# Kernel tuning notes

Measured on AMD Instinct MI355X. Metric: run time of the kernel, lower is better.

The kernel has to match this reference:

```python
import jax, jax.numpy as jnp
import numpy as np

EPS = 1e-6


def softmax_kernel_transformation(data, is_query, projection_matrix):
    # data: [B,L,H,D], projection_matrix: [M,D]
    d = data.shape[-1]
    m = projection_matrix.shape[0]
    data_normalizer = 1.0 / jnp.sqrt(jnp.sqrt(jnp.float32(d)))
    data = data_normalizer * data
    ratio = 1.0 / jnp.sqrt(jnp.float32(m))
    data_dash = jnp.einsum('blhd,md->blhm', data, projection_matrix)
    diag_data = jnp.sum(jnp.square(data), axis=-1, keepdims=True) / 2.0  # [B,L,H,1]
    if is_query:
        stab = jnp.max(data_dash, axis=-1, keepdims=True)  # per-position max over M
    else:
        stab = jnp.max(data_dash, axis=(1, 3), keepdims=True)  # max over L and M
    return ratio * (jnp.exp(data_dash - diag_data - stab) + EPS)


def causal_linear_attention(qp, kp, v):
    # qp,kp: [L,B,H,M]; v: [L,B,H,D]. Sequential prefix-sum recurrence (FAVOR+ causal).
    B, H, M = qp.shape[1], qp.shape[2], qp.shape[3]
    D = v.shape[-1]
    kv0 = jnp.zeros((B, H, M, D), dtype=v.dtype)
    ks0 = jnp.zeros((B, H, M), dtype=kp.dtype)

    def step(carry, inp):
        kv_sum, k_sum = carry
        q_t, k_t, v_t = inp  # [B,H,M], [B,H,M], [B,H,D]
        kv_sum = kv_sum + jnp.einsum('bhm,bhd->bhmd', k_t, v_t)
        k_sum = k_sum + k_t
        num_t = jnp.einsum('bhmd,bhm->bhd', kv_sum, q_t)  # numerator row
        den_t = jnp.einsum('bhm,bhm->bh', q_t, k_sum)     # normalizer row
        return (kv_sum, k_sum), (num_t, den_t)

    (_, _), (num, den) = jax.lax.scan(step, (kv0, ks0), (qp, kp, v))
    return num, den  # [L,B,H,D], [L,B,H]


def favor_attention(query, key, value, projection_matrix):
    query_prime = softmax_kernel_transformation(query, True, projection_matrix)   # [B,L,H,M]
    key_prime = softmax_kernel_transformation(key, False, projection_matrix)      # [B,L,H,M]
    qp = jnp.transpose(query_prime, (1, 0, 2, 3))  # [L,B,H,M]
    kp = jnp.transpose(key_prime, (1, 0, 2, 3))
    v = jnp.transpose(value, (1, 0, 2, 3))         # [L,B,H,D]
    num, den = causal_linear_attention(qp, kp, v)
    av = jnp.transpose(num, (1, 0, 2, 3))          # [B,L,H,D]
    norm = jnp.transpose(den, (1, 0, 2))[..., None]  # [B,L,H,1]
    return av / norm


def setup_inputs() -> dict:
    B, L, H, D, M = 2, 2048, 8, 64, 128
    root = jax.random.key(0)
    kq, kk, kv, kp = jax.random.split(root, 4)
    return {
        'query': jax.random.normal(kq, (B, L, H, D), dtype=jnp.float32),
        'key': jax.random.normal(kk, (B, L, H, D), dtype=jnp.float32),
        'value': jax.random.normal(kv, (B, L, H, D), dtype=jnp.float32),
        'projection_matrix': jax.random.normal(kp, (M, D), dtype=jnp.float32),
    }


def reference(query, key, value, projection_matrix):
    return favor_attention(query, key, value, projection_matrix)
```

## Files before the change

kernel.cpp:

```cpp
#include <hip/hip_runtime.h>
#include <math.h>

typedef __attribute__((ext_vector_type(8))) short short8;
typedef __attribute__((ext_vector_type(4))) float f32x4;
typedef __attribute__((ext_vector_type(4))) unsigned short u16x4;

constexpr int B_ = 2, L_ = 2048, H_ = 8, D_ = 64, M_ = 128;
constexpr int T_ = 64;
constexpr int C_ = L_ / T_;
constexpr float DN_ = 0.35355339059327373f;
constexpr float RATIO_ = 0.08838834764831845f;
constexpr float EPSV_ = 1e-6f;
constexpr float REPS_ = RATIO_ * EPSV_;
constexpr float KEPS_ = 64.0f * REPS_;

constexpr int XQ_ = 0, XK_ = 4608, PHO_ = 9216, VTO_ = 18432;
constexpr int QPST_ = 0, KPTO_ = 9216, KVSTO_ = 0;

__device__ inline unsigned short f2bf(float x) {
  const unsigned u = __float_as_uint(x);
  return (unsigned short)((u + 0x7fffu + ((u >> 16) & 1u)) >> 16);
}
__device__ inline float bf2f(unsigned short h) {
  return __uint_as_float(((unsigned)h) << 16);
}

__global__ __launch_bounds__(256, 3) void feat_kernel(
    const float* __restrict__ q, const float* __restrict__ k,
    const float* __restrict__ P, const float* __restrict__ v,
    unsigned short* __restrict__ qp16, unsigned short* __restrict__ kp16,
    unsigned short* __restrict__ kvc16, float* __restrict__ ksc,
    unsigned short* __restrict__ vt16, float* __restrict__ blockmax,
    float* __restrict__ vsum) {
  __shared__ __align__(16) unsigned short sm[23040];
  __shared__ float diagq_s[T_];
  __shared__ float diagk_s[T_];
  __shared__ float wred_s[2][T_];
  __shared__ float red4_s[4];

  const int sub = blockIdx.x;
  const int c = sub % C_, bh = sub / C_;
  const int b = bh >> 3, h = bh & 7;
  const int tid = threadIdx.x;
  const int w = tid >> 6, lane = tid & 63;
  const int l15 = lane & 15, l16 = lane >> 4;
  const int rblk = (w >> 1) * 32, cblk = (w & 1) * 64;

#define STAGE_X(xptr, XB, dg)                                                 \
  _Pragma("unroll") for (int it = 0; it < 4; ++it) {                          \
    const int i4 = tid + 256 * it;                                            \
    const int r = i4 >> 4, d0 = (i4 & 15) * 4;                                \
    f32x4 t4 = *reinterpret_cast<const f32x4*>(                               \
        &(xptr)[((size_t)(b * L_ + c * T_ + r) * H_ + h) * D_ + d0]);         \
    u16x4 hi;                                                                 \
    float sq = 0.f;                                                           \
    _Pragma("unroll") for (int j = 0; j < 4; ++j) {                           \
      const float xv = t4[j] * DN_;                                           \
      sq += xv * xv;                                                          \
      hi[j] = f2bf(xv);                                                       \
    }                                                                         \
    *reinterpret_cast<u16x4*>(&sm[(XB) + r * 72 + d0]) = hi;                  \
    _Pragma("unroll") for (int off = 1; off < 16; off <<= 1)                  \
        sq += __shfl_xor(sq, off, 64);                                        \
    if ((tid & 15) == 0) (dg)[r] = sq;                                        \
  }

#define DASH_MFMA(accv, XB)                                                   \
  _Pragma("unroll") for (int kk = 0; kk < 2; ++kk) {                          \
    short8 ah[2], bh8[4];                                                     \
    _Pragma("unroll") for (int ti = 0; ti < 2; ++ti)                          \
      ah[ti] = *reinterpret_cast<const short8*>(                              \
          &sm[(XB) + (rblk + ti * 16 + l15) * 72 + kk * 32 + l16 * 8]);       \
    _Pragma("unroll") for (int tj = 0; tj < 4; ++tj)                          \
      bh8[tj] = *reinterpret_cast<const short8*>(                             \
          &sm[PHO_ + (cblk + tj * 16 + l15) * 72 + kk * 32 + l16 * 8]);       \
    _Pragma("unroll") for (int ti = 0; ti < 2; ++ti)                          \
        _Pragma("unroll") for (int tj = 0; tj < 4; ++tj)                      \
            accv[ti][tj] = __builtin_amdgcn_mfma_f32_16x16x32_bf16(           \
                ah[ti], bh8[tj], accv[ti][tj], 0, 0, 0);                      \
  }

  STAGE_X(q, XQ_, diagq_s);
  STAGE_X(k, XK_, diagk_s);
  for (int i4 = tid; i4 < M_ * 16; i4 += 256) {
    const int m = i4 >> 4, d0 = (i4 & 15) * 4;
    const f32x4 t4 = *reinterpret_cast<const f32x4*>(&P[m * D_ + d0]);
    u16x4 hi;
#pragma unroll
    for (int j = 0; j < 4; ++j) hi[j] = f2bf(t4[j]);
    *reinterpret_cast<u16x4*>(&sm[PHO_ + m * 72 + d0]) = hi;
  }
#pragma unroll
  for (int it = 0; it < 4; ++it) {
    const int i4 = tid + 256 * it;
    const int t = i4 >> 4, d0 = (i4 & 15) * 4;
    const f32x4 t4 = *reinterpret_cast<const f32x4*>(
        &v[((size_t)(b * L_ + c * T_ + t) * H_ + h) * D_ + d0]);
#pragma unroll
    for (int j = 0; j < 4; ++j) sm[VTO_ + (d0 + j) * 72 + t] = f2bf(t4[j]);
  }
  __syncthreads();

  f32x4 accq[2][4], acck[2][4];
#pragma unroll
  for (int i = 0; i < 2; ++i)
#pragma unroll
    for (int j = 0; j < 4; ++j) {
      accq[i][j] = {0.f, 0.f, 0.f, 0.f};
      acck[i][j] = {0.f, 0.f, 0.f, 0.f};
    }
  DASH_MFMA(accq, XQ_);
  DASH_MFMA(acck, XK_);
  {
    float rmax[2][4];
#pragma unroll
    for (int ti = 0; ti < 2; ++ti)
#pragma unroll
      for (int j = 0; j < 4; ++j) {
        float m0 = fmaxf(fmaxf(accq[ti][0][j], accq[ti][1][j]),
                         fmaxf(accq[ti][2][j], accq[ti][3][j]));
#pragma unroll
        for (int off = 1; off < 16; off <<= 1)
          m0 = fmaxf(m0, __shfl_xor(m0, off, 64));
        rmax[ti][j] = m0;
      }
    if (l15 == 0) {
#pragma unroll
      for (int ti = 0; ti < 2; ++ti)
#pragma unroll
        for (int j = 0; j < 4; ++j)
          wred_s[w & 1][rblk + ti * 16 + l16 * 4 + j] = rmax[ti][j];
    }
  }
  {
    float bm = -INFINITY;
#pragma unroll
    for (int ti = 0; ti < 2; ++ti)
#pragma unroll
      for (int tj = 0; tj < 4; ++tj)
#pragma unroll
        for (int j = 0; j < 4; ++j) bm = fmaxf(bm, acck[ti][tj][j]);
#pragma unroll
    for (int off = 1; off < 64; off <<= 1)
      bm = fmaxf(bm, __shfl_xor(bm, off, 64));
    if (lane == 0) red4_s[w] = bm;
  }
  __syncthreads();

  const float lmax =
      fmaxf(fmaxf(red4_s[0], red4_s[1]), fmaxf(red4_s[2], red4_s[3]));
  if (tid == 0) blockmax[sub] = lmax;
#pragma unroll
  for (int ti = 0; ti < 2; ++ti)
#pragma unroll
    for (int j = 0; j < 4; ++j) {
      const int row = rblk + ti * 16 + l16 * 4 + j;
      const float sub2 =
          0.5f * diagq_s[row] + fmaxf(wred_s[0][row], wred_s[1][row]);
#pragma unroll
      for (int tj = 0; tj < 4; ++tj) {
        const int col = cblk + tj * 16 + l15;
        sm[QPST_ + row * 136 + col] =
            f2bf(RATIO_ * (expf(accq[ti][tj][j] - sub2) + EPSV_));
      }
    }
  {
    unsigned short* kpr = kp16 + ((size_t)bh * L_ + c * T_) * M_;
#pragma unroll
    for (int ti = 0; ti < 2; ++ti)
#pragma unroll
      for (int j = 0; j < 4; ++j) {
        const int row = rblk + ti * 16 + l16 * 4 + j;
        const float sub2 = 0.5f * diagk_s[row] + lmax;
#pragma unroll
        for (int tj = 0; tj < 4; ++tj) {
          const int col = cblk + tj * 16 + l15;
          const unsigned short us = f2bf(RATIO_ * expf(acck[ti][tj][j] - sub2));
          kpr[row * M_ + col] = us;
          sm[KPTO_ + col * 72 + row] = us;
        }
      }
  }
  __syncthreads();

  {
    unsigned short* outr = qp16 + ((size_t)bh * L_ + c * T_) * M_;
    for (int i8 = tid; i8 < T_ * 16; i8 += 256) {
      const int row = i8 >> 4, m0 = (i8 & 15) * 8;
      *reinterpret_cast<short8*>(&outr[row * M_ + m0]) =
          *reinterpret_cast<const short8*>(&sm[QPST_ + row * 136 + m0]);
    }
    unsigned short* vg = vt16 + (size_t)(bh * C_ + c) * (D_ * T_);
    for (int i8 = tid; i8 < D_ * 8; i8 += 256) {
      const int d = i8 >> 3, t0 = (i8 & 7) * 8;
      *reinterpret_cast<short8*>(&vg[d * T_ + t0]) =
          *reinterpret_cast<const short8*>(&sm[VTO_ + d * 72 + t0]);
    }
  }
  if (tid < M_) {
    float s = 0.f;
#pragma unroll
    for (int t8 = 0; t8 < 8; ++t8) {
      const short8 h8 =
          *reinterpret_cast<const short8*>(&sm[KPTO_ + tid * 72 + t8 * 8]);
#pragma unroll
      for (int j = 0; j < 8; ++j) s += bf2f((unsigned short)h8[j]);
    }
    ksc[(size_t)(bh * C_ + c) * M_ + tid] = s;
  }
  if (tid >= 128 && tid < 128 + D_) {
    const int d = tid - 128;
    float s = 0.f;
#pragma unroll
    for (int t8 = 0; t8 < 8; ++t8) {
      const short8 h8 =
          *reinterpret_cast<const short8*>(&sm[VTO_ + d * 72 + t8 * 8]);
#pragma unroll
      for (int j = 0; j < 8; ++j) s += bf2f((unsigned short)h8[j]);
    }
    vsum[(size_t)(bh * C_ + c) * D_ + d] = s;
  }
  f32x4 acc2[2][4];
#pragma unroll
  for (int i = 0; i < 2; ++i)
#pragma unroll
    for (int j = 0; j < 4; ++j) acc2[i][j] = {0.f, 0.f, 0.f, 0.f};
#pragma unroll
  for (int kk = 0; kk < 2; ++kk) {
    short8 av[2], bv[4];
#pragma unroll
    for (int ti = 0; ti < 2; ++ti)
      av[ti] = *reinterpret_cast<const short8*>(
          &sm[VTO_ + (rblk + ti * 16 + l15) * 72 + kk * 32 + l16 * 8]);
#pragma unroll
    for (int tj = 0; tj < 4; ++tj)
      bv[tj] = *reinterpret_cast<const short8*>(
          &sm[KPTO_ + (cblk + tj * 16 + l15) * 72 + kk * 32 + l16 * 8]);
#pragma unroll
    for (int ti = 0; ti < 2; ++ti)
#pragma unroll
      for (int tj = 0; tj < 4; ++tj)
        acc2[ti][tj] = __builtin_amdgcn_mfma_f32_16x16x32_bf16(
            av[ti], bv[tj], acc2[ti][tj], 0, 0, 0);
  }
  __syncthreads();
#pragma unroll
  for (int ti = 0; ti < 2; ++ti)
#pragma unroll
    for (int j = 0; j < 4; ++j) {
      const int row = rblk + ti * 16 + l16 * 4 + j;
#pragma unroll
      for (int tj = 0; tj < 4; ++tj) {
        const int col = cblk + tj * 16 + l15;
        sm[KVSTO_ + row * 136 + col] = f2bf(acc2[ti][tj][j]);
      }
    }
  __syncthreads();
  {
    unsigned short* ob = kvc16 + (size_t)(bh * C_ + c) * (M_ * D_);
    for (int i8 = tid; i8 < D_ * 16; i8 += 256) {
      const int d = i8 >> 4, m0 = (i8 & 15) * 8;
      *reinterpret_cast<short8*>(&ob[d * M_ + m0]) =
          *reinterpret_cast<const short8*>(&sm[KVSTO_ + d * 136 + m0]);
    }
  }
#undef STAGE_X
#undef DASH_MFMA
}

__global__ __launch_bounds__(256) void prefix_kernel(
    const unsigned short* __restrict__ kvc16,
    unsigned short* __restrict__ kvp16, float* __restrict__ ksc,
    const float* __restrict__ blockmax, const float* __restrict__ vsum) {
  __shared__ float bm_s[C_];
  __shared__ float sc_s[C_];
  __shared__ float vs_s[2][C_];
  const int bid = blockIdx.x;
  const int ej = bid & 31, bh = bid >> 5;
  if (threadIdx.x < C_) bm_s[threadIdx.x] = blockmax[bh * C_ + threadIdx.x];
  if (threadIdx.x >= 64 && threadIdx.x < 64 + 2 * C_) {
    const int t = threadIdx.x - 64;
    const int ld = t >> 5, cc = t & 31;
    vs_s[ld][cc] = vsum[(size_t)(bh * C_ + cc) * D_ + ej * 2 + ld];
  }
  __syncthreads();
  if (threadIdx.x < C_) {
    float km = -INFINITY;
#pragma unroll
    for (int cc = 0; cc < C_; ++cc) km = fmaxf(km, bm_s[cc]);
    sc_s[threadIdx.x] = expf(bm_s[threadIdx.x] - km);
  }
  __syncthreads();
  const int e = ej * 256 + threadIdx.x;
  const int dl = threadIdx.x >> 7;
  float vals[C_];
#pragma unroll
  for (int cc = 0; cc < C_; ++cc)
    vals[cc] = bf2f(kvc16[(size_t)(bh * C_ + cc) * (M_ * D_) + e]) * sc_s[cc] +
               REPS_ * vs_s[dl][cc];
  float run = 0.f;
#pragma unroll
  for (int cc = 0; cc < C_; ++cc) {
    const float t = vals[cc];
    vals[cc] = run;
    run += t;
  }
#pragma unroll
  for (int cc = 0; cc < C_; ++cc)
    kvp16[(size_t)(bh * C_ + cc) * (M_ * D_) + e] = f2bf(vals[cc]);
  if (ej == 0 && threadIdx.x < M_) {
    const int m = threadIdx.x;
    float ks[C_];
#pragma unroll
    for (int cc = 0; cc < C_; ++cc)
      ks[cc] = ksc[(size_t)(bh * C_ + cc) * M_ + m] * sc_s[cc] + KEPS_;
    float rs = 0.f;
#pragma unroll
    for (int cc = 0; cc < C_; ++cc) {
      const float t = ks[cc];
      ks[cc] = rs;
      rs += t;
    }
#pragma unroll
    for (int cc = 0; cc < C_; ++cc)
      ksc[(size_t)(bh * C_ + cc) * M_ + m] = ks[cc];
  }
}

__global__ __launch_bounds__(256, 3) void intra_kernel(
    const unsigned short* __restrict__ qp16,
    const unsigned short* __restrict__ kp16,
    const unsigned short* __restrict__ vt16,
    const unsigned short* __restrict__ kvp16, const float* __restrict__ ksp,
    const float* __restrict__ blockmax, float* __restrict__ out) {
  __shared__ __align__(16) unsigned short qp_s[T_][136];
  __shared__ __align__(16) unsigned short kp_s[T_][136];
  __shared__ __align__(16) unsigned short S_s[T_][72];
  __shared__ float ksp_s[M_];
  __shared__ float denp_s[4][T_];
  __shared__ float den_s[T_];
  __shared__ float qsum_s[T_];
  __shared__ float bm_s[C_];

  const int bid = blockIdx.x;
  const int c = bid % C_, bh = bid / C_;
  const int b = bh >> 3, h = bh & 7;
  const int tid = threadIdx.x;
  const int w = tid >> 6, lane = tid & 63;
  const int l15 = lane & 15, l16 = lane >> 4;
  const int dblk = (w & 1) * 32;

  const unsigned short* qpt = qp16 + ((size_t)bh * L_ + c * T_) * M_;
  const unsigned short* kpt = kp16 + ((size_t)bh * L_ + c * T_) * M_;
  const unsigned short* kvt = kvp16 + (size_t)(bh * C_ + c) * (M_ * D_);
  const unsigned short* vg = vt16 + (size_t)(bh * C_ + c) * (D_ * T_);

  short8 vtr[2][2], kvr[4][2];
#pragma unroll
  for (int kk = 0; kk < 2; ++kk)
#pragma unroll
    for (int tj = 0; tj < 2; ++tj)
      vtr[kk][tj] = *reinterpret_cast<const short8*>(
          &vg[(dblk + tj * 16 + l15) * T_ + kk * 32 + l16 * 8]);
#pragma unroll
  for (int kk = 0; kk < 4; ++kk)
#pragma unroll
    for (int tj = 0; tj < 2; ++tj)
      kvr[kk][tj] = *reinterpret_cast<const short8*>(
          &kvt[(dblk + tj * 16 + l15) * M_ + kk * 32 + l16 * 8]);

  if (tid < C_) bm_s[tid] = blockmax[bh * C_ + tid];
  for (int i8 = tid; i8 < T_ * 16; i8 += 256) {
    const int r = i8 >> 4, m0 = (i8 & 15) * 8;
    *reinterpret_cast<short8*>(&qp_s[r][m0]) =
        *reinterpret_cast<const short8*>(&qpt[r * M_ + m0]);
    *reinterpret_cast<short8*>(&kp_s[r][m0]) =
        *reinterpret_cast<const short8*>(&kpt[r * M_ + m0]);
  }
  if (tid < M_) ksp_s[tid] = ksp[(size_t)(bh * C_ + c) * M_ + tid];
  __syncthreads();

  {
    const int row = w * 16 + (lane >> 2), mseg = (lane & 3) * 32;
    float p = 0.f;
#pragma unroll
    for (int u = 0; u < 4; ++u) {
      const short8 h8 =
          *reinterpret_cast<const short8*>(&qp_s[row][mseg + u * 8]);
#pragma unroll
      for (int j = 0; j < 8; ++j) p += bf2f((unsigned short)h8[j]);
    }
    p += __shfl_xor(p, 1, 64);
    p += __shfl_xor(p, 2, 64);
    if ((lane & 3) == 0) qsum_s[row] = p;
  }
  __syncthreads();

  float km = -INFINITY;
#pragma unroll
  for (int cc = 0; cc < C_; ++cc) km = fmaxf(km, bm_s[cc]);
  const float sc = expf(bm_s[c] - km);

  const int rblk = (w >> 1) * 32, cblk = (w & 1) * 32;
  f32x4 Sacc[2][2];
#pragma unroll
  for (int i = 0; i < 2; ++i)
#pragma unroll
    for (int j = 0; j < 2; ++j) Sacc[i][j] = {0.f, 0.f, 0.f, 0.f};

#pragma unroll
  for (int kk = 0; kk < 4; ++kk) {
    short8 af[2], bf[2];
#pragma unroll
    for (int ti = 0; ti < 2; ++ti)
      af[ti] = *reinterpret_cast<const short8*>(
          &qp_s[rblk + ti * 16 + l15][kk * 32 + l16 * 8]);
#pragma unroll
    for (int tj = 0; tj < 2; ++tj)
      bf[tj] = *reinterpret_cast<const short8*>(
          &kp_s[cblk + tj * 16 + l15][kk * 32 + l16 * 8]);
#pragma unroll
    for (int ti = 0; ti < 2; ++ti)
#pragma unroll
      for (int tj = 0; tj < 2; ++tj)
        Sacc[ti][tj] = __builtin_amdgcn_mfma_f32_16x16x32_bf16(
            af[ti], bf[tj], Sacc[ti][tj], 0, 0, 0);
  }
#pragma unroll
  for (int ti = 0; ti < 2; ++ti)
#pragma unroll
    for (int tj = 0; tj < 2; ++tj)
#pragma unroll
      for (int j = 0; j < 4; ++j) {
        const int row = rblk + ti * 16 + l16 * 4 + j;
        const int col = cblk + tj * 16 + l15;
        const float add = REPS_ * qsum_s[row];
        const float sv = (col <= row) ? Sacc[ti][tj][j] * sc + add : 0.f;
        S_s[row][col] = f2bf(sv);
      }
  __syncthreads();

  {
    const int t = lane;
    float p = 0.f;
    if (w == 0) {
      for (int tp = 0; tp < 32; ++tp) p += bf2f(S_s[t][tp]);
    } else if (w == 1) {
      for (int tp = 32; tp < 64; ++tp) p += bf2f(S_s[t][tp]);
    } else if (w == 2) {
      for (int m = 0; m < 64; ++m) p += bf2f(qp_s[t][m]) * ksp_s[m];
    } else {
      for (int m = 64; m < 128; ++m) p += bf2f(qp_s[t][m]) * ksp_s[m];
    }
    denp_s[w][t] = p;
  }
  __syncthreads();
  if (tid < T_)
    den_s[tid] =
        denp_s[0][tid] + denp_s[1][tid] + denp_s[2][tid] + denp_s[3][tid];
  __syncthreads();

  f32x4 Nacc[2][2];
#pragma unroll
  for (int i = 0; i < 2; ++i)
#pragma unroll
    for (int j = 0; j < 2; ++j) Nacc[i][j] = {0.f, 0.f, 0.f, 0.f};

#pragma unroll
  for (int kk = 0; kk < 2; ++kk) {
    short8 af[2];
#pragma unroll
    for (int ti = 0; ti < 2; ++ti)
      af[ti] = *reinterpret_cast<const short8*>(
          &S_s[rblk + ti * 16 + l15][kk * 32 + l16 * 8]);
#pragma unroll
    for (int ti = 0; ti < 2; ++ti)
#pragma unroll
      for (int tj = 0; tj < 2; ++tj)
        Nacc[ti][tj] = __builtin_amdgcn_mfma_f32_16x16x32_bf16(
            af[ti], vtr[kk][tj], Nacc[ti][tj], 0, 0, 0);
  }
#pragma unroll
  for (int kk = 0; kk < 4; ++kk) {
    short8 af[2];
#pragma unroll
    for (int ti = 0; ti < 2; ++ti)
      af[ti] = *reinterpret_cast<const short8*>(
          &qp_s[rblk + ti * 16 + l15][kk * 32 + l16 * 8]);
#pragma unroll
    for (int ti = 0; ti < 2; ++ti)
#pragma unroll
      for (int tj = 0; tj < 2; ++tj)
        Nacc[ti][tj] = __builtin_amdgcn_mfma_f32_16x16x32_bf16(
            af[ti], kvr[kk][tj], Nacc[ti][tj], 0, 0, 0);
  }

#pragma unroll
  for (int ti = 0; ti < 2; ++ti)
#pragma unroll
    for (int j = 0; j < 4; ++j) {
      const int row = rblk + ti * 16 + l16 * 4 + j;
      const float r = 1.f / den_s[row];
      float* orow = out + ((size_t)(b * L_ + c * T_ + row) * H_ + h) * D_;
#pragma unroll
      for (int tj = 0; tj < 2; ++tj) {
        const int col = dblk + tj * 16 + l15;
        orow[col] = Nacc[ti][tj][j] * r;
      }
    }
}

extern "C" void kernel_launch(void* const* d_in, const int* in_sizes, int n_in,
                              void* d_out, int out_size, void* d_ws,
                              size_t ws_size, hipStream_t stream) {
  const float* q = (const float*)d_in[0];
  const float* k = (const float*)d_in[1];
  const float* v = (const float*)d_in[2];
  const float* P = (const float*)d_in[3];
  float* out = (float*)d_out;

  float* ws = (float*)d_ws;
  float* blockmax = ws;
  float* ksp = blockmax + 512;
  float* vsum = ksp + (size_t)B_ * H_ * C_ * M_;
  unsigned short* qp16 = (unsigned short*)(vsum + (size_t)B_ * H_ * C_ * D_);
  unsigned short* kp16 = qp16 + (size_t)B_ * H_ * L_ * M_;
  unsigned short* kvc16 = kp16 + (size_t)B_ * H_ * L_ * M_;
  unsigned short* kvp16 = kvc16 + (size_t)B_ * H_ * C_ * D_ * M_;
  unsigned short* vt16 = kvp16 + (size_t)B_ * H_ * C_ * D_ * M_;

  feat_kernel<<<B_ * H_ * C_, 256, 0, stream>>>(q, k, P, v, qp16, kp16, kvc16,
                                                ksp, vt16, blockmax, vsum);
  prefix_kernel<<<B_ * H_ * 32, 256, 0, stream>>>(kvc16, kvp16, ksp, blockmax,
                                                  vsum);
  intra_kernel<<<B_ * H_ * C_, 256, 0, stream>>>(qp16, kp16, vt16, kvp16, ksp,
                                                 blockmax, out);
}
```

Before: 41.61 us.

## Recompute query/key features in intra kernel instead of round-tripping through global memory

The feature kernel no longer computes query features or writes the bf16 qp/kp tensors to global memory. The intra kernel now reloads raw q, k and P, recomputes both projections with MFMA, applies the exponentials, and forms the per-row q sums in registers. This removes the global write and read of two L×M bf16 feature tensors per head and lets the feature kernel use less LDS with higher occupancy. In exchange, the key projection is computed twice and the intra kernel does more work and needs more LDS.

```diff
diff --git a/kernel.cpp b/kernel.cpp
--- a/kernel.cpp
+++ b/kernel.cpp
@@ -14,9 +14,6 @@
 constexpr float REPS_ = RATIO_ * EPSV_;
 constexpr float KEPS_ = 64.0f * REPS_;
 
-constexpr int XQ_ = 0, XK_ = 4608, PHO_ = 9216, VTO_ = 18432;
-constexpr int QPST_ = 0, KPTO_ = 9216, KVSTO_ = 0;
-
 __device__ inline unsigned short f2bf(float x) {
   const unsigned u = __float_as_uint(x);
   return (unsigned short)((u + 0x7fffu + ((u >> 16) & 1u)) >> 16);
@@ -25,17 +22,16 @@
   return __uint_as_float(((unsigned)h) << 16);
 }
 
-__global__ __launch_bounds__(256, 3) void feat_kernel(
-    const float* __restrict__ q, const float* __restrict__ k,
-    const float* __restrict__ P, const float* __restrict__ v,
-    unsigned short* __restrict__ qp16, unsigned short* __restrict__ kp16,
-    unsigned short* __restrict__ kvc16, float* __restrict__ ksc,
-    unsigned short* __restrict__ vt16, float* __restrict__ blockmax,
-    float* __restrict__ vsum) {
-  __shared__ __align__(16) unsigned short sm[23040];
-  __shared__ float diagq_s[T_];
+constexpr int FXK_ = 0, FPH_ = 4608, FVT_ = 13824;
+constexpr int FKPT_ = 4608, FKVST_ = 4608;
+
+__global__ __launch_bounds__(256, 4) void feat_kernel(
+    const float* __restrict__ k, const float* __restrict__ P,
+    const float* __restrict__ v, unsigned short* __restrict__ kvc16,
+    float* __restrict__ ksc, unsigned short* __restrict__ vt16,
+    float* __restrict__ blockmax, float* __restrict__ vsum) {
+  __shared__ __align__(16) unsigned short sm[18432];
   __shared__ float diagk_s[T_];
-  __shared__ float wred_s[2][T_];
   __shared__ float red4_s[4];
 
   const int sub = blockIdx.x;
@@ -46,49 +42,32 @@
   const int l15 = lane & 15, l16 = lane >> 4;
   const int rblk = (w >> 1) * 32, cblk = (w & 1) * 64;
 
-#define STAGE_X(xptr, XB, dg)                                                 \
-  _Pragma("unroll") for (int it = 0; it < 4; ++it) {                          \
-    const int i4 = tid + 256 * it;                                            \
-    const int r = i4 >> 4, d0 = (i4 & 15) * 4;                                \
-    f32x4 t4 = *reinterpret_cast<const f32x4*>(                               \
-        &(xptr)[((size_t)(b * L_ + c * T_ + r) * H_ + h) * D_ + d0]);         \
-    u16x4 hi;                                                                 \
-    float sq = 0.f;                                                           \
-    _Pragma("unroll") for (int j = 0; j < 4; ++j) {                           \
-      const float xv = t4[j] * DN_;                                           \
-      sq += xv * xv;                                                          \
-      hi[j] = f2bf(xv);                                                       \
-    }                                                                         \
-    *reinterpret_cast<u16x4*>(&sm[(XB) + r * 72 + d0]) = hi;                  \
-    _Pragma("unroll") for (int off = 1; off < 16; off <<= 1)                  \
-        sq += __shfl_xor(sq, off, 64);                                        \
-    if ((tid & 15) == 0) (dg)[r] = sq;                                        \
-  }
-
-#define DASH_MFMA(accv, XB)                                                   \
-  _Pragma("unroll") for (int kk = 0; kk < 2; ++kk) {                          \
-    short8 ah[2], bh8[4];                                                     \
-    _Pragma("unroll") for (int ti = 0; ti < 2; ++ti)                          \
-      ah[ti] = *reinterpret_cast<const short8*>(                              \
-          &sm[(XB) + (rblk + ti * 16 + l15) * 72 + kk * 32 + l16 * 8]);       \
-    _Pragma("unroll") for (int tj = 0; tj < 4; ++tj)                          \
-      bh8[tj] = *reinterpret_cast<const short8*>(                             \
-          &sm[PHO_ + (cblk + tj * 16 + l15) * 72 + kk * 32 + l16 * 8]);       \
-    _Pragma("unroll") for (int ti = 0; ti < 2; ++ti)                          \
-        _Pragma("unroll") for (int tj = 0; tj < 4; ++tj)                      \
-            accv[ti][tj] = __builtin_amdgcn_mfma_f32_16x16x32_bf16(           \
-                ah[ti], bh8[tj], accv[ti][tj], 0, 0, 0);                      \
-  }
-
-  STAGE_X(q, XQ_, diagq_s);
-  STAGE_X(k, XK_, diagk_s);
+#pragma unroll
+  for (int it = 0; it < 4; ++it) {
+    const int i4 = tid + 256 * it;
+    const int r = i4 >> 4, d0 = (i4 & 15) * 4;
+    f32x4 t4 = *reinterpret_cast<const f32x4*>(
+        &k[((size_t)(b * L_ + c * T_ + r) * H_ + h) * D_ + d0]);
+    u16x4 hi;
+    float sq = 0.f;
+#pragma unroll
+    for (int j = 0; j < 4; ++j) {
+      const float xv = t4[j] * DN_;
+      sq += xv * xv;
+      hi[j] = f2bf(xv);
+    }
+    *reinterpret_cast<u16x4*>(&sm[FXK_ + r * 72 + d0]) = hi;
+#pragma unroll
+    for (int off = 1; off < 16; off <<= 1) sq += __shfl_xor(sq, off, 64);
+    if ((tid & 15) == 0) diagk_s[r] = sq;
+  }
   for (int i4 = tid; i4 < M_ * 16; i4 += 256) {
     const int m = i4 >> 4, d0 = (i4 & 15) * 4;
     const f32x4 t4 = *reinterpret_cast<const f32x4*>(&P[m * D_ + d0]);
     u16x4 hi;
 #pragma unroll
     for (int j = 0; j < 4; ++j) hi[j] = f2bf(t4[j]);
-    *reinterpret_cast<u16x4*>(&sm[PHO_ + m * 72 + d0]) = hi;
+    *reinterpret_cast<u16x4*>(&sm[FPH_ + m * 72 + d0]) = hi;
   }
 #pragma unroll
   for (int it = 0; it < 4; ++it) {
@@ -97,40 +76,32 @@
     const f32x4 t4 = *reinterpret_cast<const f32x4*>(
         &v[((size_t)(b * L_ + c * T_ + t) * H_ + h) * D_ + d0]);
 #pragma unroll
-    for (int j = 0; j < 4; ++j) sm[VTO_ + (d0 + j) * 72 + t] = f2bf(t4[j]);
-  }
-  __syncthreads();
-
-  f32x4 accq[2][4], acck[2][4];
+    for (int j = 0; j < 4; ++j) sm[FVT_ + (d0 + j) * 72 + t] = f2bf(t4[j]);
+  }
+  __syncthreads();
+
+  f32x4 acck[2][4];
 #pragma unroll
   for (int i = 0; i < 2; ++i)
 #pragma unroll
-    for (int j = 0; j < 4; ++j) {
-      accq[i][j] = {0.f, 0.f, 0.f, 0.f};
-      acck[i][j] = {0.f, 0.f, 0.f, 0.f};
-    }
-  DASH_MFMA(accq, XQ_);
-  DASH_MFMA(acck, XK_);
-  {
-    float rmax[2][4];
-#pragma unroll
-    for (int ti = 0; ti < 2; ++ti)
-#pragma unroll
-      for (int j = 0; j < 4; ++j) {
-        float m0 = fmaxf(fmaxf(accq[ti][0][j], accq[ti][1][j]),
-                         fmaxf(accq[ti][2][j], accq[ti][3][j]));
-#pragma unroll
-        for (int off = 1; off < 16; off <<= 1)
-          m0 = fmaxf(m0, __shfl_xor(m0, off, 64));
-        rmax[ti][j] = m0;
-      }
-    if (l15 == 0) {
-#pragma unroll
-      for (int ti = 0; ti < 2; ++ti)
-#pragma unroll
-        for (int j = 0; j < 4; ++j)
-          wred_s[w & 1][rblk + ti * 16 + l16 * 4 + j] = rmax[ti][j];
-    }
+    for (int j = 0; j < 4; ++j) acck[i][j] = {0.f, 0.f, 0.f, 0.f};
+#pragma unroll
+  for (int kk = 0; kk < 2; ++kk) {
+    short8 ah[2], bh8[4];
+#pragma unroll
+    for (int ti = 0; ti < 2; ++ti)
+      ah[ti] = *reinterpret_cast<const short8*>(
+          &sm[FXK_ + (rblk + ti * 16 + l15) * 72 + kk * 32 + l16 * 8]);
+#pragma unroll
+    for (int tj = 0; tj < 4; ++tj)
+      bh8[tj] = *reinterpret_cast<const short8*>(
+          &sm[FPH_ + (cblk + tj * 16 + l15) * 72 + kk * 32 + l16 * 8]);
+#pragma unroll
+    for (int ti = 0; ti < 2; ++ti)
+#pragma unroll
+      for (int tj = 0; tj < 4; ++tj)
+        acck[ti][tj] = __builtin_amdgcn_mfma_f32_16x16x32_bf16(
+            ah[ti], bh8[tj], acck[ti][tj], 0, 0, 0);
   }
   {
     float bm = -INFINITY;
@@ -155,46 +126,44 @@
 #pragma unroll
     for (int j = 0; j < 4; ++j) {
       const int row = rblk + ti * 16 + l16 * 4 + j;
-      const float sub2 =
-          0.5f * diagq_s[row] + fmaxf(wred_s[0][row], wred_s[1][row]);
+      const float sub2 = 0.5f * diagk_s[row] + lmax;
 #pragma unroll
       for (int tj = 0; tj < 4; ++tj) {
         const int col = cblk + tj * 16 + l15;
-        sm[QPST_ + row * 136 + col] =
-            f2bf(RATIO_ * (expf(accq[ti][tj][j] - sub2) + EPSV_));
-      }
-    }
+        sm[FKPT_ + col * 72 + row] = f2bf(RATIO_ * expf(acck[ti][tj][j] - sub2));
+      }
+    }
+  __syncthreads();
+
+  f32x4 acc2[2][4];
+#pragma unroll
+  for (int i = 0; i < 2; ++i)
+#pragma unroll
+    for (int j = 0; j < 4; ++j) acc2[i][j] = {0.f, 0.f, 0.f, 0.f};
+#pragma unroll
+  for (int kk = 0; kk < 2; ++kk) {
+    short8 av[2], bv[4];
+#pragma unroll
+    for (int ti = 0; ti < 2; ++ti)
+      av[ti] = *reinterpret_cast<const short8*>(
+          &sm[FVT_ + (rblk + ti * 16 + l15) * 72 + kk * 32 + l16 * 8]);
+#pragma unroll
+    for (int tj = 0; tj < 4; ++tj)
+      bv[tj] = *reinterpret_cast<const short8*>(
+          &sm[FKPT_ + (cblk + tj * 16 + l15) * 72 + kk * 32 + l16 * 8]);
+#pragma unroll
+    for (int ti = 0; ti < 2; ++ti)
+#pragma unroll
+      for (int tj = 0; tj < 4; ++tj)
+        acc2[ti][tj] = __builtin_amdgcn_mfma_f32_16x16x32_bf16(
+            av[ti], bv[tj], acc2[ti][tj], 0, 0, 0);
+  }
   {
-    unsigned short* kpr = kp16 + ((size_t)bh * L_ + c * T_) * M_;
-#pragma unroll
-    for (int ti = 0; ti < 2; ++ti)
-#pragma unroll
-      for (int j = 0; j < 4; ++j) {
-        const int row = rblk + ti * 16 + l16 * 4 + j;
-        const float sub2 = 0.5f * diagk_s[row] + lmax;
-#pragma unroll
-        for (int tj = 0; tj < 4; ++tj) {
-          const int col = cblk + tj * 16 + l15;
-          const unsigned short us = f2bf(RATIO_ * expf(acck[ti][tj][j] - sub2));
-          kpr[row * M_ + col] = us;
-          sm[KPTO_ + col * 72 + row] = us;
-        }
-      }
-  }
-  __syncthreads();
-
-  {
-    unsigned short* outr = qp16 + ((size_t)bh * L_ + c * T_) * M_;
-    for (int i8 = tid; i8 < T_ * 16; i8 += 256) {
-      const int row = i8 >> 4, m0 = (i8 & 15) * 8;
-      *reinterpret_cast<short8*>(&outr[row * M_ + m0]) =
-          *reinterpret_cast<const short8*>(&sm[QPST_ + row * 136 + m0]);
-    }
     unsigned short* vg = vt16 + (size_t)(bh * C_ + c) * (D_ * T_);
     for (int i8 = tid; i8 < D_ * 8; i8 += 256) {
       const int d = i8 >> 3, t0 = (i8 & 7) * 8;
       *reinterpret_cast<short8*>(&vg[d * T_ + t0]) =
-          *reinterpret_cast<const short8*>(&sm[VTO_ + d * 72 + t0]);
+          *reinterpret_cast<const short8*>(&sm[FVT_ + d * 72 + t0]);
     }
   }
   if (tid < M_) {
@@ -202,7 +171,7 @@
 #pragma unroll
     for (int t8 = 0; t8 < 8; ++t8) {
       const short8 h8 =
-          *reinterpret_cast<const short8*>(&sm[KPTO_ + tid * 72 + t8 * 8]);
+          *reinterpret_cast<const short8*>(&sm[FKPT_ + tid * 72 + t8 * 8]);
 #pragma unroll
       for (int j = 0; j < 8; ++j) s += bf2f((unsigned short)h8[j]);
     }
@@ -214,34 +183,11 @@
 #pragma unroll
     for (int t8 = 0; t8 < 8; ++t8) {
       const short8 h8 =
-          *reinterpret_cast<const short8*>(&sm[VTO_ + d * 72 + t8 * 8]);
+          *reinterpret_cast<const short8*>(&sm[FVT_ + d * 72 + t8 * 8]);
 #pragma unroll
       for (int j = 0; j < 8; ++j) s += bf2f((unsigned short)h8[j]);
     }
     vsum[(size_t)(bh * C_ + c) * D_ + d] = s;
-  }
-  f32x4 acc2[2][4];
-#pragma unroll
-  for (int i = 0; i < 2; ++i)
-#pragma unroll
-    for (int j = 0; j < 4; ++j) acc2[i][j] = {0.f, 0.f, 0.f, 0.f};
-#pragma unroll
-  for (int kk = 0; kk < 2; ++kk) {
-    short8 av[2], bv[4];
-#pragma unroll
-    for (int ti = 0; ti < 2; ++ti)
-      av[ti] = *reinterpret_cast<const short8*>(
-          &sm[VTO_ + (rblk + ti * 16 + l15) * 72 + kk * 32 + l16 * 8]);
-#pragma unroll
-    for (int tj = 0; tj < 4; ++tj)
-      bv[tj] = *reinterpret_cast<const short8*>(
-          &sm[KPTO_ + (cblk + tj * 16 + l15) * 72 + kk * 32 + l16 * 8]);
-#pragma unroll
-    for (int ti = 0; ti < 2; ++ti)
-#pragma unroll
-      for (int tj = 0; tj < 4; ++tj)
-        acc2[ti][tj] = __builtin_amdgcn_mfma_f32_16x16x32_bf16(
-            av[ti], bv[tj], acc2[ti][tj], 0, 0, 0);
   }
   __syncthreads();
 #pragma unroll
@@ -252,7 +198,7 @@
 #pragma unroll
       for (int tj = 0; tj < 4; ++tj) {
         const int col = cblk + tj * 16 + l15;
-        sm[KVSTO_ + row * 136 + col] = f2bf(acc2[ti][tj][j]);
+        sm[FKVST_ + row * 136 + col] = f2bf(acc2[ti][tj][j]);
       }
     }
   __syncthreads();
@@ -261,11 +207,9 @@
     for (int i8 = tid; i8 < D_ * 16; i8 += 256) {
       const int d = i8 >> 4, m0 = (i8 & 15) * 8;
       *reinterpret_cast<short8*>(&ob[d * M_ + m0]) =
-          *reinterpret_cast<const short8*>(&sm[KVSTO_ + d * 136 + m0]);
-    }
-  }
-#undef STAGE_X
-#undef DASH_MFMA
+          *reinterpret_cast<const short8*>(&sm[FKVST_ + d * 136 + m0]);
+    }
+  }
 }
 
 __global__ __launch_bounds__(256) void prefix_kernel(
@@ -327,19 +271,22 @@
   }
 }
 
+constexpr int IXQ_ = 0, IXK_ = 4608, IPH_ = 9216;
+constexpr int IQP_ = 0, IKP_ = 9216, IS_ = 18432;
+
 __global__ __launch_bounds__(256, 3) void intra_kernel(
-    const unsigned short* __restrict__ qp16,
-    const unsigned short* __restrict__ kp16,
-    const unsigned short* __restrict__ vt16,
+    const float* __restrict__ q, const float* __restrict__ k,
+    const float* __restrict__ P, const unsigned short* __restrict__ vt16,
     const unsigned short* __restrict__ kvp16, const float* __restrict__ ksp,
     const float* __restrict__ blockmax, float* __restrict__ out) {
-  __shared__ __align__(16) unsigned short qp_s[T_][136];
-  __shared__ __align__(16) unsigned short kp_s[T_][136];
-  __shared__ __align__(16) unsigned short S_s[T_][72];
+  __shared__ __align__(16) unsigned short sm[23040];
+  __shared__ float diagq_s[T_];
+  __shared__ float diagk_s[T_];
+  __shared__ float wred_s[2][T_];
+  __shared__ float qs2_s[2][T_];
   __shared__ float ksp_s[M_];
   __shared__ float denp_s[4][T_];
   __shared__ float den_s[T_];
-  __shared__ float qsum_s[T_];
   __shared__ float bm_s[C_];
 
   const int bid = blockIdx.x;
@@ -348,13 +295,144 @@
   const int tid = threadIdx.x;
   const int w = tid >> 6, lane = tid & 63;
   const int l15 = lane & 15, l16 = lane >> 4;
+  const int rblk = (w >> 1) * 32;
+  const int cblkF = (w & 1) * 64;
+  const int cblkS = (w & 1) * 32;
   const int dblk = (w & 1) * 32;
 
-  const unsigned short* qpt = qp16 + ((size_t)bh * L_ + c * T_) * M_;
-  const unsigned short* kpt = kp16 + ((size_t)bh * L_ + c * T_) * M_;
+  if (tid < C_) bm_s[tid] = blockmax[bh * C_ + tid];
+  if (tid < M_) ksp_s[tid] = ksp[(size_t)(bh * C_ + c) * M_ + tid];
+
+#pragma unroll
+  for (int it = 0; it < 4; ++it) {
+    const int i4 = tid + 256 * it;
+    const int r = i4 >> 4, d0 = (i4 & 15) * 4;
+    f32x4 t4 = *reinterpret_cast<const f32x4*>(
+        &q[((size_t)(b * L_ + c * T_ + r) * H_ + h) * D_ + d0]);
+    u16x4 hi;
+    float sq = 0.f;
+#pragma unroll
+    for (int j = 0; j < 4; ++j) {
+      const float xv = t4[j] * DN_;
+      sq += xv * xv;
+      hi[j] = f2bf(xv);
+    }
+    *reinterpret_cast<u16x4*>(&sm[IXQ_ + r * 72 + d0]) = hi;
+#pragma unroll
+    for (int off = 1; off < 16; off <<= 1) sq += __shfl_xor(sq, off, 64);
+    if ((tid & 15) == 0) diagq_s[r] = sq;
+  }
+#pragma unroll
+  for (int it = 0; it < 4; ++it) {
+    const int i4 = tid + 256 * it;
+    const int r = i4 >> 4, d0 = (i4 & 15) * 4;
+    f32x4 t4 = *reinterpret_cast<const f32x4*>(
+        &k[((size_t)(b * L_ + c * T_ + r) * H_ + h) * D_ + d0]);
+    u16x4 hi;
+    float sq = 0.f;
+#pragma unroll
+    for (int j = 0; j < 4; ++j) {
+      const float xv = t4[j] * DN_;
+      sq += xv * xv;
+      hi[j] = f2bf(xv);
+    }
+    *reinterpret_cast<u16x4*>(&sm[IXK_ + r * 72 + d0]) = hi;
+#pragma unroll
+    for (int off = 1; off < 16; off <<= 1) sq += __shfl_xor(sq, off, 64);
+    if ((tid & 15) == 0) diagk_s[r] = sq;
+  }
+  for (int i4 = tid; i4 < M_ * 16; i4 += 256) {
+    const int m = i4 >> 4, d0 = (i4 & 15) * 4;
+    const f32x4 t4 = *reinterpret_cast<const f32x4*>(&P[m * D_ + d0]);
+    u16x4 hi;
+#pragma unroll
+    for (int j = 0; j < 4; ++j) hi[j] = f2bf(t4[j]);
+    *reinterpret_cast<u16x4*>(&sm[IPH_ + m * 72 + d0]) = hi;
+  }
+  __syncthreads();
+
+  f32x4 accq[2][4], acck[2][4];
+#pragma unroll
+  for (int i = 0; i < 2; ++i)
+#pragma unroll
+    for (int j = 0; j < 4; ++j) {
+      accq[i][j] = {0.f, 0.f, 0.f, 0.f};
+      acck[i][j] = {0.f, 0.f, 0.f, 0.f};
+    }
+#pragma unroll
+  for (int kk = 0; kk < 2; ++kk) {
+    short8 aq[2], ak[2], bh8[4];
+#pragma unroll
+    for (int ti = 0; ti < 2; ++ti) {
+      aq[ti] = *reinterpret_cast<const short8*>(
+          &sm[IXQ_ + (rblk + ti * 16 + l15) * 72 + kk * 32 + l16 * 8]);
+      ak[ti] = *reinterpret_cast<const short8*>(
+          &sm[IXK_ + (rblk + ti * 16 + l15) * 72 + kk * 32 + l16 * 8]);
+    }
+#pragma unroll
+    for (int tj = 0; tj < 4; ++tj)
+      bh8[tj] = *reinterpret_cast<const short8*>(
+          &sm[IPH_ + (cblkF + tj * 16 + l15) * 72 + kk * 32 + l16 * 8]);
+#pragma unroll
+    for (int ti = 0; ti < 2; ++ti)
+#pragma unroll
+      for (int tj = 0; tj < 4; ++tj) {
+        accq[ti][tj] = __builtin_amdgcn_mfma_f32_16x16x32_bf16(
+            aq[ti], bh8[tj], accq[ti][tj], 0, 0, 0);
+        acck[ti][tj] = __builtin_amdgcn_mfma_f32_16x16x32_bf16(
+            ak[ti], bh8[tj], acck[ti][tj], 0, 0, 0);
+      }
+  }
+  {
+    float rmax[2][4];
+#pragma unroll
+    for (int ti = 0; ti < 2; ++ti)
+#pragma unroll
+      for (int j = 0; j < 4; ++j) {
+        float m0 = fmaxf(fmaxf(accq[ti][0][j], accq[ti][1][j]),
+                         fmaxf(accq[ti][2][j], accq[ti][3][j]));
+#pragma unroll
+        for (int off = 1; off < 16; off <<= 1)
+          m0 = fmaxf(m0, __shfl_xor(m0, off, 64));
+        rmax[ti][j] = m0;
+      }
+    if (l15 == 0) {
+#pragma unroll
+      for (int ti = 0; ti < 2; ++ti)
+#pragma unroll
+        for (int j = 0; j < 4; ++j)
+          wred_s[w & 1][rblk + ti * 16 + l16 * 4 + j] = rmax[ti][j];
+    }
+  }
+  __syncthreads();
+
+  const float lmax = bm_s[c];
+#pragma unroll
+  for (int ti = 0; ti < 2; ++ti)
+#pragma unroll
+    for (int j = 0; j < 4; ++j) {
+      const int row = rblk + ti * 16 + l16 * 4 + j;
+      const float subq =
+          0.5f * diagq_s[row] + fmaxf(wred_s[0][row], wred_s[1][row]);
+      const float subk = 0.5f * diagk_s[row] + lmax;
+      float qsp = 0.f;
+#pragma unroll
+      for (int tj = 0; tj < 4; ++tj) {
+        const int col = cblkF + tj * 16 + l15;
+        const float qv = RATIO_ * (expf(accq[ti][tj][j] - subq) + EPSV_);
+        qsp += qv;
+        sm[IQP_ + row * 136 + col] = f2bf(qv);
+        sm[IKP_ + row * 136 + col] =
+            f2bf(RATIO_ * expf(acck[ti][tj][j] - subk));
+      }
+#pragma unroll
+      for (int off = 1; off < 16; off <<= 1) qsp += __shfl_xor(qsp, off, 64);
+      if (l15 == 0) qs2_s[w & 1][row] = qsp;
+    }
+  __syncthreads();
+
   const unsigned short* kvt = kvp16 + (size_t)(bh * C_ + c) * (M_ * D_);
   const unsigned short* vg = vt16 + (size_t)(bh * C_ + c) * (D_ * T_);
-
   short8 vtr[2][2], kvr[4][2];
 #pragma unroll
   for (int kk = 0; kk < 2; ++kk)
@@ -369,56 +447,27 @@
       kvr[kk][tj] = *reinterpret_cast<const short8*>(
           &kvt[(dblk + tj * 16 + l15) * M_ + kk * 32 + l16 * 8]);
 
-  if (tid < C_) bm_s[tid] = blockmax[bh * C_ + tid];
-  for (int i8 = tid; i8 < T_ * 16; i8 += 256) {
-    const int r = i8 >> 4, m0 = (i8 & 15) * 8;
-    *reinterpret_cast<short8*>(&qp_s[r][m0]) =
-        *reinterpret_cast<const short8*>(&qpt[r * M_ + m0]);
-    *reinterpret_cast<short8*>(&kp_s[r][m0]) =
-        *reinterpret_cast<const short8*>(&kpt[r * M_ + m0]);
-  }
-  if (tid < M_) ksp_s[tid] = ksp[(size_t)(bh * C_ + c) * M_ + tid];
-  __syncthreads();
-
-  {
-    const int row = w * 16 + (lane >> 2), mseg = (lane & 3) * 32;
-    float p = 0.f;
-#pragma unroll
-    for (int u = 0; u < 4; ++u) {
-      const short8 h8 =
-          *reinterpret_cast<const short8*>(&qp_s[row][mseg + u * 8]);
-#pragma unroll
-      for (int j = 0; j < 8; ++j) p += bf2f((unsigned short)h8[j]);
-    }
-    p += __shfl_xor(p, 1, 64);
-    p += __shfl_xor(p, 2, 64);
-    if ((lane & 3) == 0) qsum_s[row] = p;
-  }
-  __syncthreads();
-
   float km = -INFINITY;
 #pragma unroll
   for (int cc = 0; cc < C_; ++cc) km = fmaxf(km, bm_s[cc]);
   const float sc = expf(bm_s[c] - km);
 
-  const int rblk = (w >> 1) * 32, cblk = (w & 1) * 32;
   f32x4 Sacc[2][2];
 #pragma unroll
   for (int i = 0; i < 2; ++i)
 #pragma unroll
     for (int j = 0; j < 2; ++j) Sacc[i][j] = {0.f, 0.f, 0.f, 0.f};
-
 #pragma unroll
   for (int kk = 0; kk < 4; ++kk) {
     short8 af[2], bf[2];
 #pragma unroll
     for (int ti = 0; ti < 2; ++ti)
       af[ti] = *reinterpret_cast<const short8*>(
-          &qp_s[rblk + ti * 16 + l15][kk * 32 + l16 * 8]);
+          &sm[IQP_ + (rblk + ti * 16 + l15) * 136 + kk * 32 + l16 * 8]);
 #pragma unroll
     for (int tj = 0; tj < 2; ++tj)
       bf[tj] = *reinterpret_cast<const short8*>(
-          &kp_s[cblk + tj * 16 + l15][kk * 32 + l16 * 8]);
+          &sm[IKP_ + (cblkS + tj * 16 + l15) * 136 + kk * 32 + l16 * 8]);
 #pragma unroll
     for (int ti = 0; ti < 2; ++ti)
 #pragma unroll
@@ -433,10 +482,10 @@
 #pragma unroll
       for (int j = 0; j < 4; ++j) {
         const int row = rblk + ti * 16 + l16 * 4 + j;
-        const int col = cblk + tj * 16 + l15;
-        const float add = REPS_ * qsum_s[row];
+        const int col = cblkS + tj * 16 + l15;
+        const float add = REPS_ * (qs2_s[0][row] + qs2_s[1][row]);
         const float sv = (col <= row) ? Sacc[ti][tj][j] * sc + add : 0.f;
-        S_s[row][col] = f2bf(sv);
+        sm[IS_ + row * 72 + col] = f2bf(sv);
       }
   __syncthreads();
 
@@ -444,13 +493,15 @@
     const int t = lane;
     float p = 0.f;
     if (w == 0) {
-      for (int tp = 0; tp < 32; ++tp) p += bf2f(S_s[t][tp]);
+      for (int tp = 0; tp < 32; ++tp) p += bf2f(sm[IS_ + t * 72 + tp]);
     } else if (w == 1) {
-      for (int tp = 32; tp < 64; ++tp) p += bf2f(S_s[t][tp]);
+      for (int tp = 32; tp < 64; ++tp) p += bf2f(sm[IS_ + t * 72 + tp]);
     } else if (w == 2) {
-      for (int m = 0; m < 64; ++m) p += bf2f(qp_s[t][m]) * ksp_s[m];
+      for (int m = 0; m < 64; ++m)
+        p += bf2f(sm[IQP_ + t * 136 + m]) * ksp_s[m];
     } else {
-      for (int m = 64; m < 128; ++m) p += bf2f(qp_s[t][m]) * ksp_s[m];
+      for (int m = 64; m < 128; ++m)
+        p += bf2f(sm[IQP_ + t * 136 + m]) * ksp_s[m];
     }
     denp_s[w][t] = p;
   }
@@ -465,14 +516,13 @@
   for (int i = 0; i < 2; ++i)
 #pragma unroll
     for (int j = 0; j < 2; ++j) Nacc[i][j] = {0.f, 0.f, 0.f, 0.f};
-
 #pragma unroll
   for (int kk = 0; kk < 2; ++kk) {
     short8 af[2];
 #pragma unroll
     for (int ti = 0; ti < 2; ++ti)
       af[ti] = *reinterpret_cast<const short8*>(
-          &S_s[rblk + ti * 16 + l15][kk * 32 + l16 * 8]);
+          &sm[IS_ + (rblk + ti * 16 + l15) * 72 + kk * 32 + l16 * 8]);
 #pragma unroll
     for (int ti = 0; ti < 2; ++ti)
 #pragma unroll
@@ -486,7 +536,7 @@
 #pragma unroll
     for (int ti = 0; ti < 2; ++ti)
       af[ti] = *reinterpret_cast<const short8*>(
-          &qp_s[rblk + ti * 16 + l15][kk * 32 + l16 * 8]);
+          &sm[IQP_ + (rblk + ti * 16 + l15) * 136 + kk * 32 + l16 * 8]);
 #pragma unroll
     for (int ti = 0; ti < 2; ++ti)
 #pragma unroll
@@ -521,18 +571,16 @@
 
   float* ws = (float*)d_ws;
   float* blockmax = ws;
-  float* ksp = blockmax + 512;
-  float* vsum = ksp + (size_t)B_ * H_ * C_ * M_;
-  unsigned short* qp16 = (unsigned short*)(vsum + (size_t)B_ * H_ * C_ * D_);
-  unsigned short* kp16 = qp16 + (size_t)B_ * H_ * L_ * M_;
-  unsigned short* kvc16 = kp16 + (size_t)B_ * H_ * L_ * M_;
+  float* ksc = blockmax + 512;
+  float* vsum = ksc + (size_t)B_ * H_ * C_ * M_;
+  unsigned short* kvc16 = (unsigned short*)(vsum + (size_t)B_ * H_ * C_ * D_);
   unsigned short* kvp16 = kvc16 + (size_t)B_ * H_ * C_ * D_ * M_;
   unsigned short* vt16 = kvp16 + (size_t)B_ * H_ * C_ * D_ * M_;
 
-  feat_kernel<<<B_ * H_ * C_, 256, 0, stream>>>(q, k, P, v, qp16, kp16, kvc16,
-                                                ksp, vt16, blockmax, vsum);
-  prefix_kernel<<<B_ * H_ * 32, 256, 0, stream>>>(kvc16, kvp16, ksp, blockmax,
+  feat_kernel<<<B_ * H_ * C_, 256, 0, stream>>>(k, P, v, kvc16, ksc, vt16,
+                                                blockmax, vsum);
+  prefix_kernel<<<B_ * H_ * 32, 256, 0, stream>>>(kvc16, kvp16, ksc, blockmax,
                                                   vsum);
-  intra_kernel<<<B_ * H_ * C_, 256, 0, stream>>>(qp16, kp16, vt16, kvp16, ksp,
+  intra_kernel<<<B_ * H_ * C_, 256, 0, stream>>>(q, k, P, vt16, kvp16, ksc,
                                                  blockmax, out);
 }
```

Result: no change. 41.28 us (-0.8%).
